# Optimization experiments

Measured on AMD Instinct MI355X. Metric: run time of the kernel, lower is better.

## Reference

```python
import jax, jax.numpy as jnp
import numpy as np

B, C, T = 4, 1024, 2048
H = 16            # num_heads
G = 32            # GroupNorm groups (normalization(channels) == GroupNorm(32, C))
EPS = 1e-5


def setup_inputs() -> dict:
    key = jax.random.key(0)
    ks = jax.random.split(key, 7)
    x = jax.random.normal(ks[0], (B, C, T), dtype=jnp.float32)
    gn_scale = jax.random.normal(ks[1], (C,), dtype=jnp.float32) * 0.02 + 1.0
    gn_bias = jax.random.normal(ks[2], (C,), dtype=jnp.float32) * 0.02
    qkv_w = jax.random.normal(ks[3], (3 * C, C), dtype=jnp.float32) / np.sqrt(C)
    qkv_b = jax.random.normal(ks[4], (3 * C,), dtype=jnp.float32) * 0.02
    # NOTE: original zero-inits proj_out; randomized here so output != x for testing.
    proj_w = jax.random.normal(ks[5], (C, C), dtype=jnp.float32) / np.sqrt(C)
    proj_b = jax.random.normal(ks[6], (C,), dtype=jnp.float32) * 0.02
    return {"x": x, "gn_scale": gn_scale, "gn_bias": gn_bias,
            "qkv_w": qkv_w, "qkv_b": qkv_b, "proj_w": proj_w, "proj_b": proj_b}


def reference(x, gn_scale, gn_bias, qkv_w, qkv_b, proj_w, proj_b):
    b, c, t = x.shape
    ch = c // H
    # GroupNorm(32, C) over (channels-in-group, T)
    xg = x.reshape(b, G, c // G, t)
    mean = xg.mean(axis=(2, 3), keepdims=True)
    var = xg.var(axis=(2, 3), keepdims=True)
    xn = ((xg - mean) * jax.lax.rsqrt(var + EPS)).reshape(b, c, t)
    xn = xn * gn_scale[None, :, None] + gn_bias[None, :, None]
    # 1x1 conv QKV: [B, 3C, T]
    qkv = jnp.einsum('oc,bct->bot', qkv_w, xn) + qkv_b[None, :, None]
    q, k, v = jnp.split(qkv, 3, axis=1)
    # split heads -> [B*H, ch, T]
    q = q.reshape(b * H, ch, t)
    k = k.reshape(b * H, ch, t)
    v = v.reshape(b * H, ch, t)
    scale = 1.0 / np.sqrt(np.sqrt(ch)).astype(np.float32)
    # full T x T attention weights, softmax in fp32 (as original)
    w = jnp.einsum('bct,bcs->bts', q * scale, k * scale)
    w = jax.nn.softmax(w.astype(jnp.float32), axis=-1).astype(w.dtype)
    a = jnp.einsum('bts,bcs->bct', w, v).reshape(b, c, t)
    # 1x1 conv projection + residual
    h = jnp.einsum('oc,bct->bot', proj_w, a) + proj_b[None, :, None]
    return x + h
```

## Files before the change

kernel.cpp:

```cpp
#include <hip/hip_runtime.h>
#include <hip/hip_bf16.h>
#include <stdint.h>

#define Bn 4
#define Cn 1024
#define Tn 2048
#define Hn 16
#define Gn 32
#define SCALE_Q 0.18033688f

typedef short short8  __attribute__((ext_vector_type(8)));
typedef short short4_t __attribute__((ext_vector_type(4)));
typedef float float4_t __attribute__((ext_vector_type(4)));
typedef unsigned int uint2_t __attribute__((ext_vector_type(2)));

__device__ __forceinline__ short f2bf(float f) {
    uint32_t u = __float_as_uint(f);
    uint32_t r = (u + 0x7FFFu + ((u >> 16) & 1u)) >> 16;
    return (short)r;
}

__device__ __forceinline__ float exp2_fast(float x) {
#if __has_builtin(__builtin_amdgcn_exp2f)
    return __builtin_amdgcn_exp2f(x);
#else
    return exp2f(x);
#endif
}

__device__ __forceinline__ uint32_t pack_bf16_trunc(float lo, float hi) {
#if __has_builtin(__builtin_amdgcn_perm)
    return __builtin_amdgcn_perm(__float_as_uint(hi), __float_as_uint(lo), 0x07060302u);
#else
    return (__float_as_uint(lo) >> 16) | (__float_as_uint(hi) & 0xFFFF0000u);
#endif
}

__device__ __forceinline__ void permswap32(uint32_t& x, uint32_t& y) {
#if __has_builtin(__builtin_amdgcn_permlane32_swap)
    uint2_t r = __builtin_amdgcn_permlane32_swap(x, y, false, false);
    x = r[0]; y = r[1];
#else
    asm volatile("v_permlane32_swap_b32 %0, %1" : "+v"(x), "+v"(y));
#endif
}
__device__ __forceinline__ void permswap16(uint32_t& x, uint32_t& y) {
#if __has_builtin(__builtin_amdgcn_permlane16_swap)
    uint2_t r = __builtin_amdgcn_permlane16_swap(x, y, false, false);
    x = r[0]; y = r[1];
#else
    asm volatile("v_permlane16_swap_b32 %0, %1" : "+v"(x), "+v"(y));
#endif
}

#define GLL16(gptr, lptr)                                                      \
    __builtin_amdgcn_global_load_lds(                                          \
        (const __attribute__((address_space(1))) unsigned int*)(gptr),         \
        (__attribute__((address_space(3))) unsigned int*)(lptr), 16, 0, 0)

__global__ __launch_bounds__(256) void cvt_w(const float* __restrict__ src,
                                             short* __restrict__ dst, int n4) {
    int i = blockIdx.x * 256 + threadIdx.x;
    if (i < n4) {
        float4_t v = reinterpret_cast<const float4_t*>(src)[i];
        short4_t o;
        o[0] = f2bf(v[0]); o[1] = f2bf(v[1]); o[2] = f2bf(v[2]); o[3] = f2bf(v[3]);
        reinterpret_cast<short4_t*>(dst)[i] = o;
    }
}

__global__ __launch_bounds__(256) void groupnorm_k(const float* __restrict__ x,
                                                   const float* __restrict__ gs,
                                                   const float* __restrict__ gb,
                                                   short* __restrict__ xnT) {
    int blk = blockIdx.x;
    int b = blk >> 5, g = blk & 31;
    const float* base = x + ((size_t)(b * Cn + g * 32)) * Tn;
    int tid = threadIdx.x;

    float s = 0.f, ss = 0.f;
    const float4_t* b4 = reinterpret_cast<const float4_t*>(base);
    for (int i = tid; i < 16384; i += 256) {
        float4_t v = b4[i];
        s  += v[0] + v[1] + v[2] + v[3];
        ss += v[0]*v[0] + v[1]*v[1] + v[2]*v[2] + v[3]*v[3];
    }
    #pragma unroll
    for (int m = 1; m < 64; m <<= 1) { s += __shfl_xor(s, m); ss += __shfl_xor(ss, m); }
    __shared__ float red[8];
    int wave = tid >> 6;
    if ((tid & 63) == 0) { red[wave * 2] = s; red[wave * 2 + 1] = ss; }
    __syncthreads();
    float ts  = red[0] + red[2] + red[4] + red[6];
    float tss = red[1] + red[3] + red[5] + red[7];
    float mean = ts * (1.f / 65536.f);
    float var  = tss * (1.f / 65536.f) - mean * mean;
    float rstd = rsqrtf(var + 1e-5f);

    __shared__ float tile[64][33];
    for (int t0 = 0; t0 < Tn; t0 += 64) {
        #pragma unroll
        for (int k = 0; k < 8; k++) {
            int e = tid + k * 256;
            int c = e >> 6, tt = e & 63;
            float v = base[c * Tn + t0 + tt];
            tile[tt][c] = (v - mean) * rstd * gs[g * 32 + c] + gb[g * 32 + c];
        }
        __syncthreads();
        #pragma unroll
        for (int k = 0; k < 8; k++) {
            int f = tid + k * 256;
            int tt = f >> 5, c = f & 31;
            xnT[((size_t)(b * Tn + t0 + tt)) * Cn + g * 32 + c] = f2bf(tile[tt][c]);
        }
        __syncthreads();
    }
}

template <int MODE>
__global__ __launch_bounds__(256) void gemm_k(const short* __restrict__ W,
                                              const short* __restrict__ Bm,
                                              const float* __restrict__ bias,
                                              const float* __restrict__ xres,
                                              short* __restrict__ qkT,
                                              short* __restrict__ vbuf,
                                              float* __restrict__ outp) {
    constexpr int K = 1024;
    __shared__ short As[128 * 64];
    __shared__ short Bs[128 * 64];
    int m0 = blockIdx.x * 128, n0 = blockIdx.y * 128, b = blockIdx.z;
    int tid = threadIdx.x;
    int wave = tid >> 6, lane = tid & 63, quad = lane >> 4, l15 = lane & 15;
    int wm = wave >> 1, wn = wave & 1;
    const short* Ab = W + (size_t)m0 * K;
    const short* Bb = Bm + ((size_t)b * Tn + n0) * K;

    float4_t acc[4][4];
    float4_t z = {0.f, 0.f, 0.f, 0.f};
    #pragma unroll
    for (int i = 0; i < 4; i++)
        #pragma unroll
        for (int j = 0; j < 4; j++) acc[i][j] = z;

    int sw = l15 & 7;

    for (int k0 = 0; k0 < K; k0 += 64) {
        #pragma unroll
        for (int r = 0; r < 4; r++) {
            int cid = r * 256 + tid;
            int row = cid >> 3, j = cid & 7;
            int chunk = j ^ (row & 7);
            GLL16(Ab + (size_t)row * K + k0 + chunk * 8, As + cid * 8);
            GLL16(Bb + (size_t)row * K + k0 + chunk * 8, Bs + cid * 8);
        }
        __syncthreads();
        #pragma unroll
        for (int kk = 0; kk < 2; kk++) {
            short8 af[4], bfg[4];
            #pragma unroll
            for (int mi = 0; mi < 4; mi++)
                af[mi] = *reinterpret_cast<const short8*>(
                    &As[(wm * 64 + mi * 16 + l15) * 64 + ((4 * kk + quad) ^ sw) * 8]);
            #pragma unroll
            for (int ni = 0; ni < 4; ni++)
                bfg[ni] = *reinterpret_cast<const short8*>(
                    &Bs[(wn * 64 + ni * 16 + l15) * 64 + ((4 * kk + quad) ^ sw) * 8]);
            #pragma unroll
            for (int mi = 0; mi < 4; mi++)
                #pragma unroll
                for (int ni = 0; ni < 4; ni++)
                    acc[mi][ni] = __builtin_amdgcn_mfma_f32_16x16x32_bf16(
                        af[mi], bfg[ni], acc[mi][ni], 0, 0, 0);
        }
        __syncthreads();
    }

    if (MODE == 0) {
        #pragma unroll
        for (int mi = 0; mi < 4; mi++) {
            int mrow = m0 + wm * 64 + mi * 16 + quad * 4;
            #pragma unroll
            for (int ni = 0; ni < 4; ni++) {
                int t = n0 + wn * 64 + ni * 16 + l15;
                if (mrow < 2048) {
                    int hh = mrow >> 6, ch = mrow & 63;
                    float sc = (mrow < 1024) ? SCALE_Q : 1.0f;
                    short4_t pk;
                    #pragma unroll
                    for (int r = 0; r < 4; r++)
                        pk[r] = f2bf((acc[mi][ni][r] + bias[mrow + r]) * sc);
                    *reinterpret_cast<short4_t*>(
                        &qkT[(((size_t)b * 32 + hh) * Tn + t) * 64 + ch]) = pk;
                } else {
                    int c = mrow - 2048;
                    #pragma unroll
                    for (int r = 0; r < 4; r++)
                        vbuf[((size_t)b * Cn + c + r) * Tn + t] =
                            f2bf(acc[mi][ni][r] + bias[mrow + r]);
                }
            }
        }
    } else {
        #pragma unroll
        for (int mi = 0; mi < 4; mi++) {
            int mrow = m0 + wm * 64 + mi * 16 + quad * 4;
            #pragma unroll
            for (int ni = 0; ni < 4; ni++) {
                int t = n0 + wn * 64 + ni * 16 + l15;
                #pragma unroll
                for (int r = 0; r < 4; r++) {
                    size_t idx = ((size_t)b * Cn + mrow + r) * Tn + t;
                    outp[idx] = xres[idx] + bias[mrow + r] + acc[mi][ni][r];
                }
            }
        }
    }
}

__global__ __launch_bounds__(512, 4) void attn_k(const short* __restrict__ qkT,
                                                 const short* __restrict__ vbuf,
                                                 short* __restrict__ aT) {
    __shared__ short ks[64 * 72];
    __shared__ short vs[64 * 72];
    int bh = blockIdx.y; int b = bh >> 4, h = bh & 15;
    int t0 = blockIdx.x * 256;
    int tid = threadIdx.x;
    int wave = tid >> 6, lane = tid & 63, quad = lane >> 4, l15 = lane & 15;
    const short* qb = qkT + (((size_t)b * 32 + h) * Tn) * 64;
    const short* kb = qkT + (((size_t)b * 32 + 16 + h) * Tn) * 64;
    const short* vb = vbuf + ((size_t)b * Cn + h * 64) * Tn;
    int tw = t0 + wave * 32;

    short8 qf[2][2];
    #pragma unroll
    for (int tni = 0; tni < 2; tni++)
        #pragma unroll
        for (int kk = 0; kk < 2; kk++)
            qf[tni][kk] = *reinterpret_cast<const short8*>(
                qb + ((size_t)(tw + tni * 16 + l15)) * 64 + kk * 32 + quad * 8);

    short8 ones;
    #pragma unroll
    for (int i = 0; i < 8; i++) ones[i] = (short)0x3F80;

    float4_t z = {0.f, 0.f, 0.f, 0.f};
    float4_t acc[2][4], lacc[2];
    #pragma unroll
    for (int i = 0; i < 2; i++) {
        lacc[i] = z;
        #pragma unroll
        for (int j = 0; j < 4; j++) acc[i][j] = z;
    }

    for (int s0 = 0; s0 < Tn; s0 += 64) {
        {
            int row = tid >> 3, off = tid & 7;
            *reinterpret_cast<uint4*>(&ks[row * 72 + off * 8]) =
                *reinterpret_cast<const uint4*>(kb + ((size_t)(s0 + row)) * 64 + off * 8);
            *reinterpret_cast<uint4*>(&vs[row * 72 + off * 8]) =
                *reinterpret_cast<const uint4*>(vb + (size_t)row * Tn + s0 + off * 8);
        }
        __syncthreads();

        #pragma unroll
        for (int pr = 0; pr < 2; pr++) {
            uint32_t pk[2][2][2];
            #pragma unroll
            for (int half = 0; half < 2; half++) {
                int smi = pr * 2 + half;
                float4_t sa[2] = {z, z};
                #pragma unroll
                for (int kk = 0; kk < 2; kk++) {
                    short8 kf = *reinterpret_cast<const short8*>(
                        &ks[(smi * 16 + l15) * 72 + kk * 32 + quad * 8]);
                    #pragma unroll
                    for (int tni = 0; tni < 2; tni++)
                        sa[tni] = __builtin_amdgcn_mfma_f32_16x16x32_bf16(
                            kf, qf[tni][kk], sa[tni], 0, 0, 0);
                }
                #pragma unroll
                for (int tni = 0; tni < 2; tni++) {
                    float p0 = exp2_fast(sa[tni][0]);
                    float p1 = exp2_fast(sa[tni][1]);
                    float p2 = exp2_fast(sa[tni][2]);
                    float p3 = exp2_fast(sa[tni][3]);
                    pk[half][tni][0] = pack_bf16_trunc(p0, p1);
                    pk[half][tni][1] = pack_bf16_trunc(p2, p3);
                }
            }
            short8 vf[4];
            #pragma unroll
            for (int ci = 0; ci < 4; ci++)
                vf[ci] = *reinterpret_cast<const short8*>(
                    &vs[(ci * 16 + l15) * 72 + pr * 32 + quad * 8]);
            #pragma unroll
            for (int tni = 0; tni < 2; tni++) {
                uint32_t x0 = pk[0][tni][0], y0 = pk[1][tni][0];
                permswap32(x0, y0); permswap16(x0, y0);
                uint32_t x1 = pk[0][tni][1], y1 = pk[1][tni][1];
                permswap32(x1, y1); permswap16(x1, y1);
                uint4 afu = {x0, x1, y0, y1};
                short8 af = *reinterpret_cast<short8*>(&afu);
                lacc[tni] = __builtin_amdgcn_mfma_f32_16x16x32_bf16(
                    af, ones, lacc[tni], 0, 0, 0);
                #pragma unroll
                for (int ci = 0; ci < 4; ci++)
                    acc[tni][ci] = __builtin_amdgcn_mfma_f32_16x16x32_bf16(
                        af, vf[ci], acc[tni][ci], 0, 0, 0);
            }
        }
        __syncthreads();
    }

    #pragma unroll
    for (int tni = 0; tni < 2; tni++) {
        #pragma unroll
        for (int r = 0; r < 4; r++) {
            float rl = 1.0f / lacc[tni][r];
            int t = tw + tni * 16 + quad * 4 + r;
            #pragma unroll
            for (int ci = 0; ci < 4; ci++) {
                int ch = ci * 16 + l15;
                aT[((size_t)b * Tn + t) * Cn + h * 64 + ch] =
                    f2bf(acc[tni][ci][r] * rl);
            }
        }
    }
}

extern "C" void kernel_launch(void* const* d_in, const int* in_sizes, int n_in,
                              void* d_out, int out_size, void* d_ws, size_t ws_size,
                              hipStream_t stream) {
    const float* x     = (const float*)d_in[0];
    const float* gs    = (const float*)d_in[1];
    const float* gb    = (const float*)d_in[2];
    const float* qkvw  = (const float*)d_in[3];
    const float* qkvb  = (const float*)d_in[4];
    const float* projw = (const float*)d_in[5];
    const float* projb = (const float*)d_in[6];
    float* out = (float*)d_out;

    char* ws = (char*)d_ws;
    short* wqkv  = (short*)(ws + 0);
    short* wproj = (short*)(ws + 6291456);
    short* xnT   = (short*)(ws + 8388608);
    short* aT    = (short*)(ws + 8388608);
    short* qkT   = (short*)(ws + 25165824);
    short* vbuf  = (short*)(ws + 58720256);

    cvt_w<<<dim3(3072), dim3(256), 0, stream>>>(qkvw, wqkv, 786432);
    cvt_w<<<dim3(1024), dim3(256), 0, stream>>>(projw, wproj, 262144);
    groupnorm_k<<<dim3(Bn * Gn), dim3(256), 0, stream>>>(x, gs, gb, xnT);
    gemm_k<0><<<dim3(24, 16, 4), dim3(256), 0, stream>>>(wqkv, xnT, qkvb, nullptr,
                                                         qkT, vbuf, nullptr);
    attn_k<<<dim3(8, 64), dim3(512), 0, stream>>>(qkT, vbuf, aT);
    gemm_k<1><<<dim3(8, 16, 4), dim3(256), 0, stream>>>(wproj, aT, projb, x,
                                                        nullptr, nullptr, out);
}
```

Before: 335.3 us.

## Double-buffer K/V tiles in attention with register prefetch and MFMA priority

The attention kernel now keeps two LDS buffers for K and V. The next tile's global loads are issued into registers before the current tile is computed, then written to the alternate buffer afterwards, so each iteration needs one barrier instead of two. It also wraps the MFMA sections in s_setprio to favour matrix-issuing waves. This doubles LDS use and raises register pressure under launch_bounds(512,4), which could reduce occupancy.

```diff
diff --git a/kernel.cpp b/kernel.cpp
--- a/kernel.cpp
+++ b/kernel.cpp
@@ -220,8 +220,8 @@
 __global__ __launch_bounds__(512, 4) void attn_k(const short* __restrict__ qkT,
                                                  const short* __restrict__ vbuf,
                                                  short* __restrict__ aT) {
-    __shared__ short ks[64 * 72];
-    __shared__ short vs[64 * 72];
+    __shared__ short ks[2][64 * 72];
+    __shared__ short vs[2][64 * 72];
     int bh = blockIdx.y; int b = bh >> 4, h = bh & 15;
     int t0 = blockIdx.x * 256;
     int tid = threadIdx.x;
@@ -252,15 +252,27 @@
         for (int j = 0; j < 4; j++) acc[i][j] = z;
     }
 
-    for (int s0 = 0; s0 < Tn; s0 += 64) {
-        {
-            int row = tid >> 3, off = tid & 7;
-            *reinterpret_cast<uint4*>(&ks[row * 72 + off * 8]) =
-                *reinterpret_cast<const uint4*>(kb + ((size_t)(s0 + row)) * 64 + off * 8);
-            *reinterpret_cast<uint4*>(&vs[row * 72 + off * 8]) =
-                *reinterpret_cast<const uint4*>(vb + (size_t)row * Tn + s0 + off * 8);
-        }
-        __syncthreads();
+    int srow = tid >> 3, soff = (tid & 7) * 8;
+    const short* kgp = kb + (size_t)srow * 64 + soff;
+    const short* vgp = vb + (size_t)srow * Tn + soff;
+    short* krd = &ks[0][0]; short* kwr = &ks[1][0];
+    short* vrd = &vs[0][0]; short* vwr = &vs[1][0];
+    int sdst = srow * 72 + soff;
+
+    {
+        uint4 k0v = *reinterpret_cast<const uint4*>(kgp);
+        uint4 v0v = *reinterpret_cast<const uint4*>(vgp);
+        *reinterpret_cast<uint4*>(&krd[sdst]) = k0v;
+        *reinterpret_cast<uint4*>(&vrd[sdst]) = v0v;
+    }
+    __syncthreads();
+
+    for (int it = 0; it < Tn / 64; ++it) {
+        uint4 knx, vnx;
+        if (it < Tn / 64 - 1) {
+            knx = *reinterpret_cast<const uint4*>(kgp + (size_t)(it + 1) * 64 * 64);
+            vnx = *reinterpret_cast<const uint4*>(vgp + (size_t)(it + 1) * 64);
+        }
 
         #pragma unroll
         for (int pr = 0; pr < 2; pr++) {
@@ -269,15 +281,17 @@
             for (int half = 0; half < 2; half++) {
                 int smi = pr * 2 + half;
                 float4_t sa[2] = {z, z};
+                __builtin_amdgcn_s_setprio(1);
                 #pragma unroll
                 for (int kk = 0; kk < 2; kk++) {
                     short8 kf = *reinterpret_cast<const short8*>(
-                        &ks[(smi * 16 + l15) * 72 + kk * 32 + quad * 8]);
+                        &krd[(smi * 16 + l15) * 72 + kk * 32 + quad * 8]);
                     #pragma unroll
                     for (int tni = 0; tni < 2; tni++)
                         sa[tni] = __builtin_amdgcn_mfma_f32_16x16x32_bf16(
                             kf, qf[tni][kk], sa[tni], 0, 0, 0);
                 }
+                __builtin_amdgcn_s_setprio(0);
                 #pragma unroll
                 for (int tni = 0; tni < 2; tni++) {
                     float p0 = exp2_fast(sa[tni][0]);
@@ -292,7 +306,7 @@
             #pragma unroll
             for (int ci = 0; ci < 4; ci++)
                 vf[ci] = *reinterpret_cast<const short8*>(
-                    &vs[(ci * 16 + l15) * 72 + pr * 32 + quad * 8]);
+                    &vrd[(ci * 16 + l15) * 72 + pr * 32 + quad * 8]);
             #pragma unroll
             for (int tni = 0; tni < 2; tni++) {
                 uint32_t x0 = pk[0][tni][0], y0 = pk[1][tni][0];
@@ -301,15 +315,24 @@
                 permswap32(x1, y1); permswap16(x1, y1);
                 uint4 afu = {x0, x1, y0, y1};
                 short8 af = *reinterpret_cast<short8*>(&afu);
+                __builtin_amdgcn_s_setprio(1);
                 lacc[tni] = __builtin_amdgcn_mfma_f32_16x16x32_bf16(
                     af, ones, lacc[tni], 0, 0, 0);
                 #pragma unroll
                 for (int ci = 0; ci < 4; ci++)
                     acc[tni][ci] = __builtin_amdgcn_mfma_f32_16x16x32_bf16(
                         af, vf[ci], acc[tni][ci], 0, 0, 0);
-            }
-        }
-        __syncthreads();
+                __builtin_amdgcn_s_setprio(0);
+            }
+        }
+
+        if (it < Tn / 64 - 1) {
+            *reinterpret_cast<uint4*>(&kwr[sdst]) = knx;
+            *reinterpret_cast<uint4*>(&vwr[sdst]) = vnx;
+        }
+        __syncthreads();
+        short* tk = krd; krd = kwr; kwr = tk;
+        short* tv = vrd; vrd = vwr; vwr = tv;
     }
 
     #pragma unroll
```

New measurement: 330.5 us. About the same (-1.4%).
